# Kernel tuning notes

Measured on AMD Instinct MI355X. Metric: run time of the kernel, lower is better.

The kernel has to match this reference:

```python
import jax, jax.numpy as jnp
import numpy as np

N_HEAD, M_DIM, K_DIM, V_DIM = 16, 1024, 64, 64
LN_EPS = 1e-5


def setup_inputs() -> dict:
    key = jax.random.key(0)
    ks = jax.random.split(key, 10)
    B, L = 4, 2048
    q = jax.random.normal(ks[0], (B, L, M_DIM), dtype=jnp.float32)
    k = jax.random.normal(ks[1], (B, L, M_DIM), dtype=jnp.float32)
    v = jax.random.normal(ks[2], (B, L, M_DIM), dtype=jnp.float32)
    s = 1.0 / np.sqrt(M_DIM)
    W_qs = jax.random.normal(ks[3], (M_DIM, N_HEAD * K_DIM), dtype=jnp.float32) * s
    W_ks = jax.random.normal(ks[4], (M_DIM, N_HEAD * K_DIM), dtype=jnp.float32) * s
    W_vs = jax.random.normal(ks[5], (M_DIM, N_HEAD * V_DIM), dtype=jnp.float32) * s
    fc_w = jax.random.normal(ks[6], (N_HEAD * V_DIM, M_DIM), dtype=jnp.float32) * (1.0 / np.sqrt(N_HEAD * V_DIM))
    fc_b = jnp.zeros((M_DIM,), dtype=jnp.float32)
    ln_g = jnp.ones((M_DIM,), dtype=jnp.float32)
    ln_b = jnp.zeros((M_DIM,), dtype=jnp.float32)
    return {"q": q, "k": k, "v": v, "W_qs": W_qs, "W_ks": W_ks, "W_vs": W_vs,
            "fc_w": fc_w, "fc_b": fc_b, "ln_g": ln_g, "ln_b": ln_b}


def reference(q, k, v, W_qs, W_ks, W_vs, fc_w, fc_b, ln_g, ln_b):
    B, Lq, _ = q.shape
    residual = q
    # project and split heads: [B, L, H, D]
    qh = (q @ W_qs).reshape(B, Lq, N_HEAD, K_DIM)
    kh = (k @ W_ks).reshape(B, k.shape[1], N_HEAD, K_DIM)
    vh = (v @ W_vs).reshape(B, v.shape[1], N_HEAD, V_DIM)
    temperature = np.power(K_DIM, 0.5).astype(np.float32)
    # attention scores [B, H, Lq, Lk]
    attn = jnp.einsum('bqhd,bkhd->bhqk', qh, kh) / temperature
    attn = jax.nn.softmax(attn, axis=-1)
    out = jnp.einsum('bhqk,bkhd->bqhd', attn, vh).reshape(B, Lq, N_HEAD * V_DIM)
    out = out @ fc_w + fc_b
    x = out + residual
    mu = jnp.mean(x, axis=-1, keepdims=True)
    var = jnp.mean(jnp.square(x - mu), axis=-1, keepdims=True)
    return (x - mu) * jax.lax.rsqrt(var + LN_EPS) * ln_g + ln_b
```

## Files before the change

kernel.cpp:

```cpp
#include <hip/hip_runtime.h>
#include <math.h>

#define NHEAD 16
#define MDIM  1024
#define KD    64
#define BATCH 4
#define SEQ   2048
#define MROWS (BATCH*SEQ)

using short8 = __attribute__((ext_vector_type(8))) short;
using f4     = __attribute__((ext_vector_type(4))) float;
using f16x   = __attribute__((ext_vector_type(16))) float;

__device__ inline short f2bf(float x) {
  union { float f; unsigned u; } v; v.f = x;
  unsigned r = v.u + 0x7fffu + ((v.u >> 16) & 1u);
  return (short)(r >> 16);
}

__device__ __forceinline__ float fast_exp2(float x) {
#if __has_builtin(__builtin_amdgcn_exp2f)
  return __builtin_amdgcn_exp2f(x);
#else
  return exp2f(x);
#endif
}

__device__ __forceinline__ int pack_bf16(float lo, float hi) {
#if __has_builtin(__builtin_amdgcn_cvt_pk_bf16_f32)
  auto t = __builtin_amdgcn_cvt_pk_bf16_f32(lo, hi);
  int r; __builtin_memcpy(&r, &t, 4); return r;
#else
  unsigned u0 = __float_as_uint(lo) + 0x8000u;
  unsigned u1 = __float_as_uint(hi) + 0x8000u;
  return (int)__builtin_amdgcn_perm(u1, u0, 0x07060302u);
#endif
}

__device__ __forceinline__ void g2l16(const void* g, void* l) {
  __builtin_amdgcn_global_load_lds((const __attribute__((address_space(1))) unsigned int*)g,
                                   (__attribute__((address_space(3))) unsigned int*)l, 16, 0, 0);
}

#define AHIP_WAIT_LGKM0 asm volatile("s_waitcnt lgkmcnt(0)" ::: "memory")
#define AHIP_WAIT_VM8   asm volatile("s_waitcnt vmcnt(8)" ::: "memory")
#define AHIP_WAIT_VM0   asm volatile("s_waitcnt vmcnt(0)" ::: "memory")
#define AHIP_SFENCE     __builtin_amdgcn_sched_barrier(0)
#define AHIP_BAR        __builtin_amdgcn_s_barrier()

__global__ void wtrans_kernel(const float* __restrict__ w0, const float* __restrict__ w1,
                              const float* __restrict__ w2, const float* __restrict__ w3,
                              short* __restrict__ o0, short* __restrict__ o1,
                              short* __restrict__ o2, short* __restrict__ o3) {
  int z = blockIdx.z;
  const float* in = z == 0 ? w0 : (z == 1 ? w1 : (z == 2 ? w2 : w3));
  short* out = z == 0 ? o0 : (z == 1 ? o1 : (z == 2 ? o2 : o3));
  __shared__ float t[32][33];
  int bx = blockIdx.x * 32, by = blockIdx.y * 32;
  int tx = threadIdx.x, ty = threadIdx.y;
#pragma unroll
  for (int i = 0; i < 4; i++)
    t[ty + i * 8][tx] = in[(size_t)(by + ty + i * 8) * MDIM + bx + tx];
  __syncthreads();
#pragma unroll
  for (int i = 0; i < 4; i++)
    out[(size_t)(bx + ty + i * 8) * MDIM + by + tx] = f2bf(t[tx][ty + i * 8]);
}

__global__ void cvt_kernel(const float* __restrict__ q, const float* __restrict__ k,
                           const float* __restrict__ v, short* __restrict__ qb,
                           short* __restrict__ kb, short* __restrict__ vb) {
  const float* in = blockIdx.y == 0 ? q : (blockIdx.y == 1 ? k : v);
  short* out = blockIdx.y == 0 ? qb : (blockIdx.y == 1 ? kb : vb);
  size_t i = (size_t)blockIdx.x * 256 + threadIdx.x;
  float4 a = ((const float4*)in)[2 * i];
  float4 b = ((const float4*)in)[2 * i + 1];
  short8 s = {f2bf(a.x), f2bf(a.y), f2bf(a.z), f2bf(a.w),
              f2bf(b.x), f2bf(b.y), f2bf(b.z), f2bf(b.w)};
  ((short8*)out)[i] = s;
}

#define G4_PROLOGUE(Ab, Bt)                                                            \
  int tid = threadIdx.x, wid = tid >> 6, lane = tid & 63;                              \
  int quad = lane >> 4, low = lane & 15;                                               \
  int l8 = lane & 7, lr = lane >> 3;                                                   \
  int wrow = (wid >> 1) * 64, wcol = (wid & 1) * 64;                                   \
  const short* aS = Ab + (size_t)(m0 + wid * 32 + lr) * 1024 + (l8 ^ lr) * 8;          \
  const short* bS = Bt + (size_t)(n0 + wid * 32 + lr) * 1024 + (l8 ^ lr) * 8;          \
  auto stage = [&](int t, int b) {                                                     \
    const short* a = aS + t * 64;                                                      \
    const short* bb = bS + t * 64;                                                     \
    short* ad = &As[b][wid * 2048];                                                    \
    short* bd = &Bs[b][wid * 2048];                                                    \
    g2l16(a, ad);                                                                      \
    g2l16(a + 8 * 1024, ad + 512);                                                     \
    g2l16(a + 16 * 1024, ad + 1024);                                                   \
    g2l16(a + 24 * 1024, ad + 1536);                                                   \
    g2l16(bb, bd);                                                                     \
    g2l16(bb + 8 * 1024, bd + 512);                                                    \
    g2l16(bb + 16 * 1024, bd + 1024);                                                  \
    g2l16(bb + 24 * 1024, bd + 1536);                                                  \
  };                                                                                   \
  f4 acc[4][4];                                                                        \
  _Pragma("unroll")                                                                    \
  for (int mf = 0; mf < 4; mf++)                                                       \
    _Pragma("unroll")                                                                  \
    for (int nf = 0; nf < 4; nf++) {                                                   \
      acc[mf][nf][0] = 0.f; acc[mf][nf][1] = 0.f;                                      \
      acc[mf][nf][2] = 0.f; acc[mf][nf][3] = 0.f;                                      \
    }                                                                                  \
  stage(0, 0);                                                                         \
  stage(1, 1);                                                                         \
  AHIP_WAIT_VM8; AHIP_SFENCE; AHIP_BAR; AHIP_SFENCE;

#define G4_MAIN_LOOP()                                                                 \
  for (int t = 0; t < 16; ++t) {                                                       \
    const int cur = t & 1;                                                             \
    short8 af[2][4], bfv[2][4];                                                        \
    _Pragma("unroll")                                                                  \
    for (int kk = 0; kk < 2; kk++) {                                                   \
      _Pragma("unroll")                                                                \
      for (int mf = 0; mf < 4; mf++)                                                   \
        af[kk][mf] = *(const short8*)&As[cur][(wrow + mf * 16 + low) * 64 +            \
                                              (((kk * 4 + quad) ^ (low & 7)) * 8)];    \
      _Pragma("unroll")                                                                \
      for (int nf = 0; nf < 4; nf++)                                                   \
        bfv[kk][nf] = *(const short8*)&Bs[cur][(wcol + nf * 16 + low) * 64 +           \
                                               (((kk * 4 + quad) ^ (low & 7)) * 8)];   \
    }                                                                                  \
    AHIP_WAIT_LGKM0; AHIP_SFENCE;                                                      \
    AHIP_BAR; AHIP_SFENCE;                                                             \
    if (t + 2 < 16) stage(t + 2, cur);                                                 \
    __builtin_amdgcn_s_setprio(1);                                                     \
    _Pragma("unroll")                                                                  \
    for (int kk = 0; kk < 2; kk++)                                                     \
      _Pragma("unroll")                                                                \
      for (int mf = 0; mf < 4; mf++)                                                   \
        _Pragma("unroll")                                                              \
        for (int nf = 0; nf < 4; nf++)                                                 \
          acc[mf][nf] = __builtin_amdgcn_mfma_f32_16x16x32_bf16(af[kk][mf],            \
                          bfv[kk][nf], acc[mf][nf], 0, 0, 0);                          \
    __builtin_amdgcn_s_setprio(0);                                                     \
    AHIP_SFENCE;                                                                       \
    if (t + 2 < 16) { AHIP_WAIT_VM8; } else { AHIP_WAIT_VM0; }                         \
    AHIP_SFENCE; AHIP_BAR; AHIP_SFENCE;                                                \
  }

__launch_bounds__(256, 2)
__global__ void gemm_qkv_kernel(const short* __restrict__ qb, const short* __restrict__ kb,
                                const short* __restrict__ vb, const short* __restrict__ Wqt,
                                const short* __restrict__ Wkt, const short* __restrict__ Wvt,
                                short* __restrict__ Qh, short* __restrict__ Kh,
                                short* __restrict__ Vt) {
  __shared__ __attribute__((aligned(16))) short As[2][128 * 64];
  __shared__ __attribute__((aligned(16))) short Bs[2][128 * 64];
  int z = blockIdx.z;
  const short* Ab = z == 0 ? qb : (z == 1 ? kb : vb);
  const short* Bt = z == 0 ? Wqt : (z == 1 ? Wkt : Wvt);
  int m0 = blockIdx.x * 128, n0 = blockIdx.y * 128;

  G4_PROLOGUE(Ab, Bt)
  G4_MAIN_LOOP()

  float scale = z == 0 ? 0.18033688011112042f : 1.0f;
  short* dst = z == 0 ? Qh : (z == 1 ? Kh : Vt);
#pragma unroll
  for (int mf = 0; mf < 4; mf++)
#pragma unroll
    for (int nf = 0; nf < 4; nf++)
#pragma unroll
      for (int r2 = 0; r2 < 4; r2++) {
        int gr = m0 + wrow + mf * 16 + quad * 4 + r2;
        int gc = n0 + wcol + nf * 16 + low;
        float val = acc[mf][nf][r2];
        int b = gr >> 11, l = gr & 2047, h = gc >> 6, d = gc & 63;
        if (z < 2)
          dst[(((size_t)(b * NHEAD + h)) * SEQ + l) * KD + d] = f2bf(val * scale);
        else
          dst[(((size_t)(b * NHEAD + h)) * KD + d) * SEQ + l] = f2bf(val);
      }
}

__launch_bounds__(256, 2)
__global__ void gemm_fc_kernel(const short* __restrict__ Ab, const short* __restrict__ Bt,
                               float* __restrict__ dst, const float* __restrict__ bias,
                               const float* __restrict__ res) {
  __shared__ __attribute__((aligned(16))) short As[2][128 * 64];
  __shared__ __attribute__((aligned(16))) short Bs[2][128 * 64];
  int m0 = blockIdx.x * 128, n0 = blockIdx.y * 128;

  G4_PROLOGUE(Ab, Bt)
  G4_MAIN_LOOP()

#pragma unroll
  for (int mf = 0; mf < 4; mf++)
#pragma unroll
    for (int nf = 0; nf < 4; nf++)
#pragma unroll
      for (int r2 = 0; r2 < 4; r2++) {
        int gr = m0 + wrow + mf * 16 + quad * 4 + r2;
        int gc = n0 + wcol + nf * 16 + low;
        dst[(size_t)gr * 1024 + gc] = acc[mf][nf][r2] + bias[gc] + res[(size_t)gr * 1024 + gc];
      }
}

__launch_bounds__(512, 4)
__global__ void attn_kernel(const short* __restrict__ Qh, const short* __restrict__ Kh,
                            const short* __restrict__ Vt, short* __restrict__ Out) {
  __shared__ __attribute__((aligned(16))) short KT[2][128 * 64];
  __shared__ __attribute__((aligned(16))) short VT[2][64 * 128];
  int tid = threadIdx.x;
  int wave = tid >> 6, lane = tid & 63;
  int l = lane & 31, hi = lane >> 5;
  int bx = blockIdx.x, by = blockIdx.y;
  int bh = bx + (by & 7) * 8;
  int qc = by >> 3;
  int q0 = qc * 256 + wave * 32;

  const short* Qb = Qh + (size_t)bh * SEQ * KD;
  const short* Kb = Kh + (size_t)bh * SEQ * KD;
  const short* Vb = Vt + (size_t)bh * KD * SEQ;

  int srowK = lane >> 3;
  int schK = (lane & 7) ^ srowK;
  const short* kS0 = Kb + (size_t)(wave * 16 + srowK) * KD + schK * 8;
  const short* kS1 = kS0 + (size_t)8 * KD;
  int srowV = lane >> 4;
  int rV0 = wave * 8 + srowV;
  int schV0 = (lane & 15) ^ (rV0 & 15);
  int schV1 = (lane & 15) ^ ((rV0 + 4) & 15);
  const short* vS0 = Vb + (size_t)rV0 * SEQ + schV0 * 8;
  const short* vS1 = Vb + (size_t)(rV0 + 4) * SEQ + schV1 * 8;

  auto stage = [&](int k0, int b) {
    g2l16(kS0 + (size_t)k0 * KD, &KT[b][wave * 1024]);
    g2l16(kS1 + (size_t)k0 * KD, &KT[b][wave * 1024 + 512]);
    g2l16(vS0 + k0, &VT[b][wave * 1024]);
    g2l16(vS1 + k0, &VT[b][wave * 1024 + 512]);
  };

  short8 qf[4];
#pragma unroll
  for (int ks = 0; ks < 4; ks++)
    qf[ks] = *(const short8*)&Qb[(size_t)(q0 + l) * KD + ks * 16 + hi * 8];

  f16x Oacc[2], lacc, fz;
#pragma unroll
  for (int i = 0; i < 16; i++) { Oacc[0][i] = 0.f; Oacc[1][i] = 0.f; lacc[i] = 0.f; fz[i] = 0.f; }
  const short8 onesb = {0x3F80, 0x3F80, 0x3F80, 0x3F80, 0x3F80, 0x3F80, 0x3F80, 0x3F80};

  stage(0, 0);
  __syncthreads();

  for (int c = 0; c < SEQ / 128; c++) {
    int b = c & 1;
    if (c + 1 < SEQ / 128) stage((c + 1) * 128, b ^ 1);

#pragma unroll
    for (int nt = 0; nt < 4; nt++) {
      short8 kf[4];
#pragma unroll
      for (int ks = 0; ks < 4; ks++)
        kf[ks] = *(const short8*)&KT[b][(nt * 32 + l) * 64 + (((ks * 2 + hi) ^ (l & 7)) * 8)];

      f16x S;
      __builtin_amdgcn_s_setprio(1);
      S = __builtin_amdgcn_mfma_f32_32x32x16_bf16(kf[0], qf[0], fz, 0, 0, 0);
      S = __builtin_amdgcn_mfma_f32_32x32x16_bf16(kf[1], qf[1], S, 0, 0, 0);
      S = __builtin_amdgcn_mfma_f32_32x32x16_bf16(kf[2], qf[2], S, 0, 0, 0);
      S = __builtin_amdgcn_mfma_f32_32x32x16_bf16(kf[3], qf[3], S, 0, 0, 0);
      __builtin_amdgcn_s_setprio(0);

      int u[8];
#pragma unroll
      for (int i = 0; i < 8; i++)
        u[i] = pack_bf16(fast_exp2(S[2 * i]), fast_exp2(S[2 * i + 1]));
      asm("v_permlane32_swap_b32 %0, %1" : "+v"(u[0]), "+v"(u[2]));
      asm("v_permlane32_swap_b32 %0, %1" : "+v"(u[1]), "+v"(u[3]));
      asm("v_permlane32_swap_b32 %0, %1" : "+v"(u[4]), "+v"(u[6]));
      asm("v_permlane32_swap_b32 %0, %1" : "+v"(u[5]), "+v"(u[7]));
      short8 pa0, pa1;
      {
        int t0[4] = {u[0], u[1], u[2], u[3]};
        int t1[4] = {u[4], u[5], u[6], u[7]};
        __builtin_memcpy(&pa0, t0, 16);
        __builtin_memcpy(&pa1, t1, 16);
      }

      __builtin_amdgcn_s_setprio(1);
      lacc = __builtin_amdgcn_mfma_f32_32x32x16_bf16(pa0, onesb, lacc, 0, 0, 0);
      lacc = __builtin_amdgcn_mfma_f32_32x32x16_bf16(pa1, onesb, lacc, 0, 0, 0);

#pragma unroll
      for (int dt = 0; dt < 2; dt++) {
        short8 vf0 = *(const short8*)&VT[b][(dt * 32 + l) * 128 + (((nt * 4 + 0 + hi) ^ (l & 15)) * 8)];
        short8 vf1 = *(const short8*)&VT[b][(dt * 32 + l) * 128 + (((nt * 4 + 2 + hi) ^ (l & 15)) * 8)];
        Oacc[dt] = __builtin_amdgcn_mfma_f32_32x32x16_bf16(pa0, vf0, Oacc[dt], 0, 0, 0);
        Oacc[dt] = __builtin_amdgcn_mfma_f32_32x32x16_bf16(pa1, vf1, Oacc[dt], 0, 0, 0);
      }
      __builtin_amdgcn_s_setprio(0);
    }
    __syncthreads();
  }

  int bb = bh >> 4, h = bh & 15;
#pragma unroll
  for (int r = 0; r < 16; r++) {
    int qrow = q0 + (r & 3) + 8 * (r >> 2) + 4 * hi;
    float iv = 1.0f / lacc[r];
#pragma unroll
    for (int dt = 0; dt < 2; dt++) {
      size_t idx = ((size_t)(bb * SEQ + qrow)) * 1024 + h * 64 + dt * 32 + l;
      Out[idx] = f2bf(Oacc[dt][r] * iv);
    }
  }
}

__launch_bounds__(256)
__global__ void ln_kernel(const float* __restrict__ x, const float* __restrict__ g,
                          const float* __restrict__ b, float* __restrict__ out) {
  int row = blockIdx.x, tid = threadIdx.x;
  const float4* xr = (const float4*)(x + (size_t)row * 1024);
  float4 v = xr[tid];
  float s = v.x + v.y + v.z + v.w;
  float q = v.x * v.x + v.y * v.y + v.z * v.z + v.w * v.w;
#pragma unroll
  for (int o = 32; o > 0; o >>= 1) { s += __shfl_xor(s, o); q += __shfl_xor(q, o); }
  __shared__ float ss[4], sq[4];
  if ((tid & 63) == 0) { ss[tid >> 6] = s; sq[tid >> 6] = q; }
  __syncthreads();
  if (tid == 0) {
    float S = ss[0] + ss[1] + ss[2] + ss[3];
    float Q = sq[0] + sq[1] + sq[2] + sq[3];
    float mean = S * (1.f / 1024.f);
    float var = Q * (1.f / 1024.f) - mean * mean;
    ss[0] = mean; sq[0] = rsqrtf(var + 1e-5f);
  }
  __syncthreads();
  float mean = ss[0], rs = sq[0];
  const float4* g4 = (const float4*)g;
  const float4* b4 = (const float4*)b;
  float4 gg = g4[tid], bb = b4[tid], o;
  o.x = (v.x - mean) * rs * gg.x + bb.x;
  o.y = (v.y - mean) * rs * gg.y + bb.y;
  o.z = (v.z - mean) * rs * gg.z + bb.z;
  o.w = (v.w - mean) * rs * gg.w + bb.w;
  ((float4*)(out + (size_t)row * 1024))[tid] = o;
}

extern "C" void kernel_launch(void* const* d_in, const int* in_sizes, int n_in,
                              void* d_out, int out_size, void* d_ws, size_t ws_size,
                              hipStream_t stream) {
  const float* q   = (const float*)d_in[0];
  const float* k   = (const float*)d_in[1];
  const float* v   = (const float*)d_in[2];
  const float* Wq  = (const float*)d_in[3];
  const float* Wk  = (const float*)d_in[4];
  const float* Wv  = (const float*)d_in[5];
  const float* fcw = (const float*)d_in[6];
  const float* fcb = (const float*)d_in[7];
  const float* lng = (const float*)d_in[8];
  const float* lnb = (const float*)d_in[9];
  float* out = (float*)d_out;

  char* ws = (char*)d_ws;
  const size_t MB = 1024 * 1024;
  short* Wqt = (short*)(ws + 0 * MB);
  short* Wkt = (short*)(ws + 2 * MB);
  short* Wvt = (short*)(ws + 4 * MB);
  short* fct = (short*)(ws + 6 * MB);
  short* qb  = (short*)(ws + 8 * MB);
  short* kb  = (short*)(ws + 24 * MB);
  short* vb  = (short*)(ws + 40 * MB);
  short* Kh  = (short*)(ws + 8 * MB);
  short* Vt  = (short*)(ws + 24 * MB);
  short* Ao  = (short*)(ws + 40 * MB);
  short* Qh  = (short*)(ws + 56 * MB);
  float* X   = (float*)(ws + 8 * MB);

  wtrans_kernel<<<dim3(32, 32, 4), dim3(32, 8), 0, stream>>>(Wq, Wk, Wv, fcw, Wqt, Wkt, Wvt, fct);

  cvt_kernel<<<dim3(MROWS * MDIM / 8 / 256, 3), 256, 0, stream>>>(q, k, v, qb, kb, vb);

  gemm_qkv_kernel<<<dim3(64, 8, 3), 256, 0, stream>>>(qb, kb, vb, Wqt, Wkt, Wvt, Qh, Kh, Vt);

  attn_kernel<<<dim3(8, 64), 512, 0, stream>>>(Qh, Kh, Vt, Ao);

  gemm_fc_kernel<<<dim3(64, 8), 256, 0, stream>>>(Ao, fct, X, fcb, q);

  ln_kernel<<<MROWS, 256, 0, stream>>>(X, lng, lnb, out);
}
```

Measured before the change: 345.9 us.

## Fuse fp32-to-bf16 activation conversion into QKV GEMM A-tile staging

Removes the separate conversion kernel and has the QKV GEMM load fp32 activations directly into registers, convert them with packed bf16 instructions, and write them to LDS, while B tiles still use direct global-to-LDS loads. This drops a full write and read of the bf16 copies of q, k and v (about 100MB of traffic) and one kernel launch. In exchange, each of the 8 column blocks re-reads its A rows as fp32, which doubles the A-side bytes per tile, and the kernel needs more registers and VALU work inside the pipelined loop.

```diff
diff --git a/kernel.cpp b/kernel.cpp
--- a/kernel.cpp
+++ b/kernel.cpp
@@ -16,6 +16,10 @@
   union { float f; unsigned u; } v; v.f = x;
   unsigned r = v.u + 0x7fffu + ((v.u >> 16) & 1u);
   return (short)(r >> 16);
+}
+
+__device__ __forceinline__ int cvtpk(float lo, float hi) {
+  int r; asm("v_cvt_pk_bf16_f32 %0, %1, %2" : "=v"(r) : "v"(lo), "v"(hi)); return r;
 }
 
 __device__ __forceinline__ float fast_exp2(float x) {
@@ -43,6 +47,7 @@
 }
 
 #define AHIP_WAIT_LGKM0 asm volatile("s_waitcnt lgkmcnt(0)" ::: "memory")
+#define AHIP_WAIT_VM4   asm volatile("s_waitcnt vmcnt(4)" ::: "memory")
 #define AHIP_WAIT_VM8   asm volatile("s_waitcnt vmcnt(8)" ::: "memory")
 #define AHIP_WAIT_VM0   asm volatile("s_waitcnt vmcnt(0)" ::: "memory")
 #define AHIP_SFENCE     __builtin_amdgcn_sched_barrier(0)
@@ -65,19 +70,6 @@
 #pragma unroll
   for (int i = 0; i < 4; i++)
     out[(size_t)(bx + ty + i * 8) * MDIM + by + tx] = f2bf(t[tx][ty + i * 8]);
-}
-
-__global__ void cvt_kernel(const float* __restrict__ q, const float* __restrict__ k,
-                           const float* __restrict__ v, short* __restrict__ qb,
-                           short* __restrict__ kb, short* __restrict__ vb) {
-  const float* in = blockIdx.y == 0 ? q : (blockIdx.y == 1 ? k : v);
-  short* out = blockIdx.y == 0 ? qb : (blockIdx.y == 1 ? kb : vb);
-  size_t i = (size_t)blockIdx.x * 256 + threadIdx.x;
-  float4 a = ((const float4*)in)[2 * i];
-  float4 b = ((const float4*)in)[2 * i + 1];
-  short8 s = {f2bf(a.x), f2bf(a.y), f2bf(a.z), f2bf(a.w),
-              f2bf(b.x), f2bf(b.y), f2bf(b.z), f2bf(b.w)};
-  ((short8*)out)[i] = s;
 }
 
 #define G4_PROLOGUE(Ab, Bt)                                                            \
@@ -147,20 +139,115 @@
   }
 
 __launch_bounds__(256, 2)
-__global__ void gemm_qkv_kernel(const short* __restrict__ qb, const short* __restrict__ kb,
-                                const short* __restrict__ vb, const short* __restrict__ Wqt,
+__global__ void gemm_qkv_kernel(const float* __restrict__ qf32, const float* __restrict__ kf32,
+                                const float* __restrict__ vf32, const short* __restrict__ Wqt,
                                 const short* __restrict__ Wkt, const short* __restrict__ Wvt,
                                 short* __restrict__ Qh, short* __restrict__ Kh,
                                 short* __restrict__ Vt) {
   __shared__ __attribute__((aligned(16))) short As[2][128 * 64];
   __shared__ __attribute__((aligned(16))) short Bs[2][128 * 64];
   int z = blockIdx.z;
-  const short* Ab = z == 0 ? qb : (z == 1 ? kb : vb);
+  const float* Af = z == 0 ? qf32 : (z == 1 ? kf32 : vf32);
   const short* Bt = z == 0 ? Wqt : (z == 1 ? Wkt : Wvt);
   int m0 = blockIdx.x * 128, n0 = blockIdx.y * 128;
-
-  G4_PROLOGUE(Ab, Bt)
-  G4_MAIN_LOOP()
+  int tid = threadIdx.x, wid = tid >> 6, lane = tid & 63;
+  int quad = lane >> 4, low = lane & 15;
+  int l8 = lane & 7, lr = lane >> 3;
+  int sch = l8 ^ lr;
+  int wrow = (wid >> 1) * 64, wcol = (wid & 1) * 64;
+  const float* aF = Af + (size_t)(m0 + wid * 32 + lr) * 1024 + sch * 8;
+  const short* bS = Bt + (size_t)(n0 + wid * 32 + lr) * 1024 + sch * 8;
+
+  auto stageB = [&](int t, int b) {
+    const short* bb = bS + t * 64;
+    short* bd = &Bs[b][wid * 2048];
+    g2l16(bb, bd);
+    g2l16(bb + 8 * 1024, bd + 512);
+    g2l16(bb + 16 * 1024, bd + 1024);
+    g2l16(bb + 24 * 1024, bd + 1536);
+  };
+
+  f4 acc[4][4];
+#pragma unroll
+  for (int mf = 0; mf < 4; mf++)
+#pragma unroll
+    for (int nf = 0; nf < 4; nf++) {
+      acc[mf][nf][0] = 0.f; acc[mf][nf][1] = 0.f;
+      acc[mf][nf][2] = 0.f; acc[mf][nf][3] = 0.f;
+    }
+
+#pragma unroll
+  for (int t0 = 0; t0 < 2; ++t0) {
+    float4 va[4][2];
+#pragma unroll
+    for (int i = 0; i < 4; i++) {
+      const float4* p = (const float4*)(aF + (size_t)(8 * i) * 1024 + t0 * 64);
+      va[i][0] = p[0]; va[i][1] = p[1];
+    }
+    stageB(t0, t0);
+#pragma unroll
+    for (int i = 0; i < 4; i++) {
+      int4 w = {cvtpk(va[i][0].x, va[i][0].y), cvtpk(va[i][0].z, va[i][0].w),
+                cvtpk(va[i][1].x, va[i][1].y), cvtpk(va[i][1].z, va[i][1].w)};
+      *(int4*)&As[t0][wid * 2048 + i * 512 + lane * 8] = w;
+    }
+  }
+  AHIP_WAIT_VM0; AHIP_WAIT_LGKM0; AHIP_SFENCE; AHIP_BAR; AHIP_SFENCE;
+
+  for (int t = 0; t < 16; ++t) {
+    const int cur = t & 1;
+    short8 af[2][4], bfv[2][4];
+#pragma unroll
+    for (int kk = 0; kk < 2; kk++) {
+#pragma unroll
+      for (int mf = 0; mf < 4; mf++)
+        af[kk][mf] = *(const short8*)&As[cur][(wrow + mf * 16 + low) * 64 +
+                                             (((kk * 4 + quad) ^ (low & 7)) * 8)];
+#pragma unroll
+      for (int nf = 0; nf < 4; nf++)
+        bfv[kk][nf] = *(const short8*)&Bs[cur][(wcol + nf * 16 + low) * 64 +
+                                              (((kk * 4 + quad) ^ (low & 7)) * 8)];
+    }
+    AHIP_WAIT_LGKM0; AHIP_SFENCE;
+    AHIP_BAR; AHIP_SFENCE;
+
+    float4 va[4][2];
+    if (t + 2 < 16) {
+#pragma unroll
+      for (int i = 0; i < 4; i++) {
+        const float4* p = (const float4*)(aF + (size_t)(8 * i) * 1024 + (t + 2) * 64);
+        va[i][0] = p[0]; va[i][1] = p[1];
+      }
+      stageB(t + 2, cur);
+    }
+    AHIP_SFENCE;
+
+    __builtin_amdgcn_s_setprio(1);
+#pragma unroll
+    for (int kk = 0; kk < 2; kk++)
+#pragma unroll
+      for (int mf = 0; mf < 4; mf++)
+#pragma unroll
+        for (int nf = 0; nf < 4; nf++)
+          acc[mf][nf] = __builtin_amdgcn_mfma_f32_16x16x32_bf16(af[kk][mf],
+                          bfv[kk][nf], acc[mf][nf], 0, 0, 0);
+    __builtin_amdgcn_s_setprio(0);
+    AHIP_SFENCE;
+
+    if (t + 2 < 16) {
+#pragma unroll
+      for (int i = 0; i < 4; i++) {
+        int4 w = {cvtpk(va[i][0].x, va[i][0].y), cvtpk(va[i][0].z, va[i][0].w),
+                  cvtpk(va[i][1].x, va[i][1].y), cvtpk(va[i][1].z, va[i][1].w)};
+        *(int4*)&As[cur][wid * 2048 + i * 512 + lane * 8] = w;
+      }
+      AHIP_SFENCE;
+      AHIP_WAIT_VM4;
+    } else {
+      AHIP_WAIT_VM0;
+    }
+    AHIP_SFENCE; AHIP_BAR; AHIP_SFENCE;
+  }
 
   float scale = z == 0 ? 0.18033688011112042f : 1.0f;
   short* dst = z == 0 ? Qh : (z == 1 ? Kh : Vt);
@@ -369,9 +456,6 @@
   short* Wkt = (short*)(ws + 2 * MB);
   short* Wvt = (short*)(ws + 4 * MB);
   short* fct = (short*)(ws + 6 * MB);
-  short* qb  = (short*)(ws + 8 * MB);
-  short* kb  = (short*)(ws + 24 * MB);
-  short* vb  = (short*)(ws + 40 * MB);
   short* Kh  = (short*)(ws + 8 * MB);
   short* Vt  = (short*)(ws + 24 * MB);
   short* Ao  = (short*)(ws + 40 * MB);
@@ -380,9 +464,7 @@
 
   wtrans_kernel<<<dim3(32, 32, 4), dim3(32, 8), 0, stream>>>(Wq, Wk, Wv, fcw, Wqt, Wkt, Wvt, fct);
 
-  cvt_kernel<<<dim3(MROWS * MDIM / 8 / 256, 3), 256, 0, stream>>>(q, k, v, qb, kb, vb);
-
-  gemm_qkv_kernel<<<dim3(64, 8, 3), 256, 0, stream>>>(qb, kb, vb, Wqt, Wkt, Wvt, Qh, Kh, Vt);
+  gemm_qkv_kernel<<<dim3(64, 8, 3), 256, 0, stream>>>(q, k, v, Wqt, Wkt, Wvt, Qh, Kh, Vt);
 
   attn_kernel<<<dim3(8, 64), 512, 0, stream>>>(Qh, Kh, Vt, Ao);
 
```

Result: slower. 354.1 us (+2.4%).
